# Optimization experiments

Hardware: AMD Instinct MI355X
Metric: run time of the kernel (lower is better)

Reference implementation:

```python
import jax, jax.numpy as jnp
import numpy as np

B, I, H = 4096, 512, 1024


def setup_inputs() -> dict:
    key = jax.random.key(0)
    ks = jax.random.split(key, 22)
    inp = {
        "y": jax.random.normal(ks[0], (B, I), jnp.float32),
        "h_light": jax.random.normal(ks[1], (B, H), jnp.float32),
        "c_light": jax.random.normal(ks[2], (B, H), jnp.float32),
        "h_temp": jax.random.normal(ks[3], (B, H), jnp.float32),
        "c_temp": jax.random.normal(ks[4], (B, H), jnp.float32),
    }
    names = ["w_f_light", "w_i_light", "w_c_light", "w_o_light",
             "w_f_light_temp", "w_i_light_temp", "w_c_light_temp", "w_o_light_temp"]
    for j, n in enumerate(names):
        inp[n] = jax.random.normal(ks[5 + j], (H, H + I), jnp.float32) * 0.02
        inp["b" + n[1:]] = jax.random.normal(ks[13 + j], (H,), jnp.float32) * 0.02
    return inp


def _branch(hx, wf, bf, wi, bi, wc, bc, wo, bo):
    # Fuse the 4 gate GEMMs of one branch into a single [B, H+I] x [H+I, 4H] matmul
    W = jnp.concatenate([wf, wi, wc, wo], axis=0)            # [4H, H+I]
    b = jnp.concatenate([bf, bi, bc, bo], axis=0)            # [4H]
    z = hx @ W.T + b                                         # [B, 4H]
    zf, zi, zc, zo = jnp.split(z, 4, axis=1)
    return jax.nn.sigmoid(zf), jax.nn.sigmoid(zi), jnp.tanh(zc), jax.nn.sigmoid(zo)


def reference(y, h_light, c_light, h_temp, c_temp,
              w_f_light, b_f_light, w_i_light, b_i_light,
              w_c_light, b_c_light, w_o_light, b_o_light,
              w_f_light_temp, b_f_light_temp, w_i_light_temp, b_i_light_temp,
              w_c_light_temp, b_c_light_temp, w_o_light_temp, b_o_light_temp):
    hx_l = jnp.concatenate([h_light, y], axis=1)  # [B, H+I]
    hx_t = jnp.concatenate([h_temp, y], axis=1)   # [B, H+I]
    f1, i1, ch1, o1 = _branch(hx_l, w_f_light, b_f_light, w_i_light, b_i_light,
                              w_c_light, b_c_light, w_o_light, b_o_light)
    f2, i2, ch2, o2 = _branch(hx_t, w_f_light_temp, b_f_light_temp, w_i_light_temp,
                              b_i_light_temp, w_c_light_temp, b_c_light_temp,
                              w_o_light_temp, b_o_light_temp)
    c_new = (f1 * c_light + i1 * ch1) + (f2 * c_light + i2 * ch2)
    h_new = (o1 + o2) * jnp.tanh(c_new)
    return h_new, c_new
```

## Files before the change

kernel.cpp:

```cpp
#include <hip/hip_runtime.h>
#include <stdint.h>


#define B_DIM 4096
#define I_DIM 512
#define H_DIM 1024
#define K_DIM 1536

typedef __attribute__((ext_vector_type(8))) __bf16 bf16x8;
typedef __attribute__((ext_vector_type(4))) float f32x4;
typedef __attribute__((ext_vector_type(4))) uint32_t u32x4;

static __device__ __forceinline__ uint32_t f2bf(float f) {
  uint32_t u = __builtin_bit_cast(uint32_t, f);
  return (u + 0x7FFFu + ((u >> 16) & 1u)) >> 16;
}
static __device__ __forceinline__ uint32_t pack2(float lo, float hi) {
  return f2bf(lo) | (f2bf(hi) << 16);
}
static __device__ __forceinline__ float sigf(float x) {
  return 1.f / (1.f + __expf(-x));
}
static __device__ __forceinline__ float tanhfast(float x) {
  float t = __expf(fminf(2.f * x, 80.f));
  return (t - 1.f) / (t + 1.f);
}

__global__ __launch_bounds__(256) void convert_kernel(
    const float* __restrict__ y, const float* __restrict__ h_light,
    const float* __restrict__ h_temp,
    const float* __restrict__ w0, const float* __restrict__ w1,
    const float* __restrict__ w2, const float* __restrict__ w3,
    const float* __restrict__ w4, const float* __restrict__ w5,
    const float* __restrict__ w6, const float* __restrict__ w7,
    uint16_t* __restrict__ ws)
{
  const int CPR = K_DIM / 8;
  const int A_CHUNKS = 2 * B_DIM * CPR;
  const int TOT = A_CHUNKS + 8 * H_DIM * CPR;
  for (int chunk = blockIdx.x * 256 + threadIdx.x; chunk < TOT;
       chunk += gridDim.x * 256) {
    int row_all = chunk / CPR;
    int cs = chunk - row_all * CPR;
    int cl = (cs & ~7) | ((cs & 7) ^ (row_all & 7));
    int k0 = cl * 8;
    const float* src;
    if (chunk < A_CHUNKS) {
      int branch = row_all >> 12;
      int row = row_all & (B_DIM - 1);
      const float* hb = branch ? h_temp : h_light;
      src = (k0 < H_DIM) ? (hb + (size_t)row * H_DIM + k0)
                         : (y + (size_t)row * I_DIM + (k0 - H_DIM));
    } else {
      int ra = row_all - 2 * B_DIM;
      int mat = ra >> 10;
      int row = ra & (H_DIM - 1);
      const float* w = (mat < 4) ? ((mat < 2) ? (mat == 0 ? w0 : w1) : (mat == 2 ? w2 : w3))
                                 : ((mat < 6) ? (mat == 4 ? w4 : w5) : (mat == 6 ? w6 : w7));
      src = w + (size_t)row * K_DIM + k0;
    }
    f32x4 v0 = *(const f32x4*)src;
    f32x4 v1 = *(const f32x4*)(src + 4);
    u32x4 o;
    o[0] = pack2(v0[0], v0[1]);
    o[1] = pack2(v0[2], v0[3]);
    o[2] = pack2(v1[0], v1[1]);
    o[3] = pack2(v1[2], v1[3]);
    *(u32x4*)(ws + (size_t)chunk * 8) = o;
  }
}

__global__ __launch_bounds__(512, 2) void lstm_fused_kernel(
    const uint16_t* __restrict__ ws,
    const float* __restrict__ c_light,
    const float* __restrict__ bf1, const float* __restrict__ bi1,
    const float* __restrict__ bc1, const float* __restrict__ bo1,
    const float* __restrict__ bf2, const float* __restrict__ bi2,
    const float* __restrict__ bc2, const float* __restrict__ bo2,
    float* __restrict__ out)
{
  __shared__ alignas(128) char smem[96 * 1024];

  const int tid = threadIdx.x;
  const int lane = tid & 63;
  const int wv = tid >> 6;

  int bid = blockIdx.x;
  int wg = (bid & 7) * 64 + (bid >> 3);
  const int bm0 = (wg >> 4) * 128;
  const int bn0 = (wg & 15) * 64;

  const uint16_t* wsA = ws;
  const uint16_t* wsW = ws + (size_t)2 * B_DIM * K_DIM;

  const int rA = lane & 15;
  const int kg = lane >> 4;
  const int swz = rA & 7;
  const int branch = wv >> 2;
  const char* As = smem + branch * 16384;
  const char* Bs = smem + 32768 + wv * 8192;

  f32x4 acc[8][4];
#pragma unroll
  for (int m = 0; m < 8; ++m)
#pragma unroll
    for (int n = 0; n < 4; ++n) acc[m][n] = (f32x4){0.f, 0.f, 0.f, 0.f};

  for (int kt = 0; kt < K_DIM / 64; ++kt) {
    __syncthreads();
#pragma unroll
    for (int i = 0; i < 12; ++i) {
      int chunk = i * 512 + tid;
      const uint16_t* src;
      if (chunk < 2048) {
        int br = chunk >> 10;
        int r = (chunk >> 3) & 127;
        int c = chunk & 7;
        src = wsA + (size_t)br * (B_DIM * K_DIM) + (size_t)(bm0 + r) * K_DIM + kt * 64 + c * 8;
      } else {
        int cb2 = chunk - 2048;
        int mt = cb2 >> 9;
        int r = (cb2 >> 3) & 63;
        int c = cb2 & 7;
        src = wsW + (size_t)mt * (H_DIM * K_DIM) + (size_t)(bn0 + r) * K_DIM + kt * 64 + c * 8;
      }
      __builtin_amdgcn_global_load_lds(
          (const __attribute__((address_space(1))) void*)src,
          (__attribute__((address_space(3))) void*)(smem + chunk * 16),
          16, 0, 0);
    }
    asm volatile("s_waitcnt vmcnt(0)" ::: "memory");
    __syncthreads();

#pragma unroll
    for (int kk = 0; kk < 2; ++kk) {
      const int cs = (kk * 4 + kg) ^ swz;
      bf16x8 a[8];
      bf16x8 b[4];
#pragma unroll
      for (int m = 0; m < 8; ++m)
        a[m] = *(const bf16x8*)(As + (m * 16 + rA) * 128 + cs * 16);
#pragma unroll
      for (int n = 0; n < 4; ++n)
        b[n] = *(const bf16x8*)(Bs + (n * 16 + rA) * 128 + cs * 16);
#pragma unroll
      for (int m = 0; m < 8; ++m)
#pragma unroll
        for (int n = 0; n < 4; ++n)
          acc[m][n] = __builtin_amdgcn_mfma_f32_16x16x32_bf16(a[m], b[n], acc[m][n], 0, 0, 0);
    }
  }

  float* zst = (float*)smem;
#pragma unroll
  for (int q = 0; q < 4; ++q) {
    __syncthreads();
#pragma unroll
    for (int mm = 0; mm < 2; ++mm)
#pragma unroll
      for (int n = 0; n < 4; ++n)
#pragma unroll
        for (int j = 0; j < 4; ++j) {
          int r = mm * 16 + kg * 4 + j;
          int c = n * 16 + rA;
          zst[wv * 2176 + r * 68 + c] = acc[q * 2 + mm][n][j];
        }
    __syncthreads();

    int r = tid >> 4;
    int cb = (tid & 15) * 4;
    int grow = bm0 + q * 32 + r;
    int gc = bn0 + cb;
    const float* zb = zst + r * 68 + cb;
    f32x4 z0 = *(const f32x4*)(zb + 0 * 2176) + *(const f32x4*)(bf1 + gc);
    f32x4 z1 = *(const f32x4*)(zb + 1 * 2176) + *(const f32x4*)(bi1 + gc);
    f32x4 z2 = *(const f32x4*)(zb + 2 * 2176) + *(const f32x4*)(bc1 + gc);
    f32x4 z3 = *(const f32x4*)(zb + 3 * 2176) + *(const f32x4*)(bo1 + gc);
    f32x4 z4 = *(const f32x4*)(zb + 4 * 2176) + *(const f32x4*)(bf2 + gc);
    f32x4 z5 = *(const f32x4*)(zb + 5 * 2176) + *(const f32x4*)(bi2 + gc);
    f32x4 z6 = *(const f32x4*)(zb + 6 * 2176) + *(const f32x4*)(bc2 + gc);
    f32x4 z7 = *(const f32x4*)(zb + 7 * 2176) + *(const f32x4*)(bo2 + gc);
    f32x4 cl4 = *(const f32x4*)(c_light + (size_t)grow * H_DIM + gc);
    f32x4 hv, cv;
#pragma unroll
    for (int j = 0; j < 4; ++j) {
      float f1 = sigf(z0[j]);
      float i1 = sigf(z1[j]);
      float ch1 = tanhfast(z2[j]);
      float o1 = sigf(z3[j]);
      float f2 = sigf(z4[j]);
      float i2 = sigf(z5[j]);
      float ch2 = tanhfast(z6[j]);
      float o2 = sigf(z7[j]);
      float cn = f1 * cl4[j] + i1 * ch1 + f2 * cl4[j] + i2 * ch2;
      hv[j] = (o1 + o2) * tanhfast(cn);
      cv[j] = cn;
    }
    *(f32x4*)(out + (size_t)grow * H_DIM + gc) = hv;
    *(f32x4*)(out + (size_t)(B_DIM * H_DIM) + (size_t)grow * H_DIM + gc) = cv;
  }
}

extern "C" void kernel_launch(void* const* d_in, const int* in_sizes, int n_in,
                              void* d_out, int out_size, void* d_ws, size_t ws_size,
                              hipStream_t stream) {
  (void)in_sizes; (void)n_in; (void)out_size; (void)ws_size;
  const float* y       = (const float*)d_in[0];
  const float* h_light = (const float*)d_in[1];
  const float* c_light = (const float*)d_in[2];
  const float* h_temp  = (const float*)d_in[3];
  uint16_t* ws = (uint16_t*)d_ws;

  convert_kernel<<<2048, 256, 0, stream>>>(
      y, h_light, h_temp,
      (const float*)d_in[5],  (const float*)d_in[7],  (const float*)d_in[9],  (const float*)d_in[11],
      (const float*)d_in[13], (const float*)d_in[15], (const float*)d_in[17], (const float*)d_in[19],
      ws);

  lstm_fused_kernel<<<512, 512, 0, stream>>>(
      ws, c_light,
      (const float*)d_in[6],  (const float*)d_in[8],  (const float*)d_in[10], (const float*)d_in[12],
      (const float*)d_in[14], (const float*)d_in[16], (const float*)d_in[18], (const float*)d_in[20],
      (float*)d_out);
}
```

Baseline: 328.1 us.

## Triple-buffer K tiles with interleaved async prefetch and split MFMA phases

The GEMM main loop now uses a 3-stage LDS ring with 32-wide K tiles. Prefetch loads for tile kt+2 are spread across two MFMA phases, and barriers plus s_setprio are used so loads overlap compute, replacing the old load-all, wait, then compute loop. The LDS swizzle is changed to match the 64-byte row layout. The convert kernel is simplified to one block per row with 192 threads. The extra LDS buffer (144KB total) and more barriers per tile may reduce occupancy relative to the launch bound of two blocks.

Result: faster. 303.1 us (-7.6%).

```diff
diff --git a/kernel.cpp b/kernel.cpp
--- a/kernel.cpp
+++ b/kernel.cpp
@@ -6,6 +6,8 @@
 #define I_DIM 512
 #define H_DIM 1024
 #define K_DIM 1536
+#define NK 48
+#define BUFB (48 * 1024)
 
 typedef __attribute__((ext_vector_type(8))) __bf16 bf16x8;
 typedef __attribute__((ext_vector_type(4))) float f32x4;
@@ -26,7 +28,7 @@
   return (t - 1.f) / (t + 1.f);
 }
 
-__global__ __launch_bounds__(256) void convert_kernel(
+__global__ __launch_bounds__(192) void convert_kernel(
     const float* __restrict__ y, const float* __restrict__ h_light,
     const float* __restrict__ h_temp,
     const float* __restrict__ w0, const float* __restrict__ w1,
@@ -35,39 +37,33 @@
     const float* __restrict__ w6, const float* __restrict__ w7,
     uint16_t* __restrict__ ws)
 {
-  const int CPR = K_DIM / 8;
-  const int A_CHUNKS = 2 * B_DIM * CPR;
-  const int TOT = A_CHUNKS + 8 * H_DIM * CPR;
-  for (int chunk = blockIdx.x * 256 + threadIdx.x; chunk < TOT;
-       chunk += gridDim.x * 256) {
-    int row_all = chunk / CPR;
-    int cs = chunk - row_all * CPR;
-    int cl = (cs & ~7) | ((cs & 7) ^ (row_all & 7));
-    int k0 = cl * 8;
-    const float* src;
-    if (chunk < A_CHUNKS) {
-      int branch = row_all >> 12;
-      int row = row_all & (B_DIM - 1);
-      const float* hb = branch ? h_temp : h_light;
-      src = (k0 < H_DIM) ? (hb + (size_t)row * H_DIM + k0)
-                         : (y + (size_t)row * I_DIM + (k0 - H_DIM));
-    } else {
-      int ra = row_all - 2 * B_DIM;
-      int mat = ra >> 10;
-      int row = ra & (H_DIM - 1);
-      const float* w = (mat < 4) ? ((mat < 2) ? (mat == 0 ? w0 : w1) : (mat == 2 ? w2 : w3))
-                                 : ((mat < 6) ? (mat == 4 ? w4 : w5) : (mat == 6 ? w6 : w7));
-      src = w + (size_t)row * K_DIM + k0;
-    }
-    f32x4 v0 = *(const f32x4*)src;
-    f32x4 v1 = *(const f32x4*)(src + 4);
-    u32x4 o;
-    o[0] = pack2(v0[0], v0[1]);
-    o[1] = pack2(v0[2], v0[3]);
-    o[2] = pack2(v1[0], v1[1]);
-    o[3] = pack2(v1[2], v1[3]);
-    *(u32x4*)(ws + (size_t)chunk * 8) = o;
-  }
+  const int row_all = blockIdx.x;
+  const int cs = threadIdx.x;
+  const int cl = (cs & ~3) | ((cs & 3) ^ ((row_all >> 1) & 3));
+  const int k0 = cl * 8;
+  const float* src;
+  if (row_all < 2 * B_DIM) {
+    const int branch = row_all >> 12;
+    const int row = row_all & (B_DIM - 1);
+    const float* hb = branch ? h_temp : h_light;
+    src = (k0 < H_DIM) ? (hb + (size_t)row * H_DIM + k0)
+                       : (y + (size_t)row * I_DIM + (k0 - H_DIM));
+  } else {
+    const int ra = row_all - 2 * B_DIM;
+    const int mat = ra >> 10;
+    const int row = ra & (H_DIM - 1);
+    const float* w = (mat < 4) ? ((mat < 2) ? (mat == 0 ? w0 : w1) : (mat == 2 ? w2 : w3))
+                               : ((mat < 6) ? (mat == 4 ? w4 : w5) : (mat == 6 ? w6 : w7));
+    src = w + (size_t)row * K_DIM + k0;
+  }
+  f32x4 v0 = *(const f32x4*)src;
+  f32x4 v1 = *(const f32x4*)(src + 4);
+  u32x4 o;
+  o[0] = pack2(v0[0], v0[1]);
+  o[1] = pack2(v0[2], v0[3]);
+  o[2] = pack2(v1[0], v1[1]);
+  o[3] = pack2(v1[2], v1[3]);
+  *(u32x4*)(ws + ((size_t)row_all * 192 + cs) * 8) = o;
 }
 
 __global__ __launch_bounds__(512, 2) void lstm_fused_kernel(
@@ -79,14 +75,14 @@
     const float* __restrict__ bc2, const float* __restrict__ bo2,
     float* __restrict__ out)
 {
-  __shared__ alignas(128) char smem[96 * 1024];
+  __shared__ alignas(128) char smem[3 * BUFB];
 
   const int tid = threadIdx.x;
   const int lane = tid & 63;
   const int wv = tid >> 6;
 
-  int bid = blockIdx.x;
-  int wg = (bid & 7) * 64 + (bid >> 3);
+  const int bid = blockIdx.x;
+  const int wg = (bid & 7) * 64 + (bid >> 3);
   const int bm0 = (wg >> 4) * 128;
   const int bn0 = (wg & 15) * 64;
 
@@ -95,10 +91,37 @@
 
   const int rA = lane & 15;
   const int kg = lane >> 4;
-  const int swz = rA & 7;
-  const int branch = wv >> 2;
-  const char* As = smem + branch * 16384;
-  const char* Bs = smem + 32768 + wv * 8192;
+  const uint32_t fo = (uint32_t)rA * 64u + (uint32_t)((kg ^ ((rA >> 1) & 3))) * 16u;
+
+  const uint16_t* sA0;
+  const uint16_t* sA1;
+  const uint16_t* sB[4];
+  {
+    int c = tid;
+    sA0 = wsA + (size_t)(bm0 + ((c >> 2) & 127)) * K_DIM + (c & 3) * 8;
+    c = 512 + tid;
+    sA1 = wsA + (size_t)B_DIM * K_DIM + (size_t)(bm0 + ((c >> 2) & 127)) * K_DIM + (c & 3) * 8;
+#pragma unroll
+    for (int j = 0; j < 4; ++j) {
+      int c2 = j * 512 + tid;
+      sB[j] = wsW + (size_t)(c2 >> 8) * ((size_t)H_DIM * K_DIM) +
+              (size_t)(bn0 + ((c2 >> 2) & 63)) * K_DIM + (c2 & 3) * 8;
+    }
+  }
+  const uint32_t ldA0 = (uint32_t)tid * 16u;
+  const uint32_t ldA1 = (uint32_t)(512 + tid) * 16u;
+  uint32_t ldB[4];
+#pragma unroll
+  for (int j = 0; j < 4; ++j) ldB[j] = (uint32_t)(1024 + j * 512 + tid) * 16u;
+
+  const uint32_t aBase = (uint32_t)(wv >> 2) * 8192u;
+  const uint32_t bBase = 16384u + (uint32_t)wv * 4096u;
+
+#define ISSUE(srcp, ldsoff, tg)                                              \
+  __builtin_amdgcn_global_load_lds(                                          \
+      (const __attribute__((address_space(1))) void*)(srcp),                 \
+      (__attribute__((address_space(3))) void*)(&smem[(size_t)(tg)*BUFB + (ldsoff)]), \
+      16, 0, 0)
 
   f32x4 acc[8][4];
 #pragma unroll
@@ -106,50 +129,64 @@
 #pragma unroll
     for (int n = 0; n < 4; ++n) acc[m][n] = (f32x4){0.f, 0.f, 0.f, 0.f};
 
-  for (int kt = 0; kt < K_DIM / 64; ++kt) {
-    __syncthreads();
-#pragma unroll
-    for (int i = 0; i < 12; ++i) {
-      int chunk = i * 512 + tid;
-      const uint16_t* src;
-      if (chunk < 2048) {
-        int br = chunk >> 10;
-        int r = (chunk >> 3) & 127;
-        int c = chunk & 7;
-        src = wsA + (size_t)br * (B_DIM * K_DIM) + (size_t)(bm0 + r) * K_DIM + kt * 64 + c * 8;
-      } else {
-        int cb2 = chunk - 2048;
-        int mt = cb2 >> 9;
-        int r = (cb2 >> 3) & 63;
-        int c = cb2 & 7;
-        src = wsW + (size_t)mt * (H_DIM * K_DIM) + (size_t)(bn0 + r) * K_DIM + kt * 64 + c * 8;
-      }
-      __builtin_amdgcn_global_load_lds(
-          (const __attribute__((address_space(1))) void*)src,
-          (__attribute__((address_space(3))) void*)(smem + chunk * 16),
-          16, 0, 0);
-    }
-    asm volatile("s_waitcnt vmcnt(0)" ::: "memory");
-    __syncthreads();
-
-#pragma unroll
-    for (int kk = 0; kk < 2; ++kk) {
-      const int cs = (kk * 4 + kg) ^ swz;
-      bf16x8 a[8];
-      bf16x8 b[4];
-#pragma unroll
-      for (int m = 0; m < 8; ++m)
-        a[m] = *(const bf16x8*)(As + (m * 16 + rA) * 128 + cs * 16);
+  ISSUE(sA0, ldA0, 0); ISSUE(sA1, ldA1, 0);
+#pragma unroll
+  for (int j = 0; j < 4; ++j) ISSUE(sB[j], ldB[j], 0);
+  ISSUE(sA0 + 32, ldA0, 1); ISSUE(sA1 + 32, ldA1, 1);
+#pragma unroll
+  for (int j = 0; j < 4; ++j) ISSUE(sB[j] + 32, ldB[j], 1);
+  sA0 += 64; sA1 += 64;
+#pragma unroll
+  for (int j = 0; j < 4; ++j) sB[j] += 64;
+  asm volatile("s_waitcnt vmcnt(6)" ::: "memory");
+  __builtin_amdgcn_s_barrier();
+
+  for (int kt = 0; kt < NK; ++kt) {
+    const int bi = kt % 3;
+    const int tg = (bi == 0) ? 2 : bi - 1;
+    const char* As = smem + (size_t)bi * BUFB + aBase;
+    const char* Bs = smem + (size_t)bi * BUFB + bBase;
+    const bool pf = (kt + 2 < NK);
+
+    bf16x8 Af[4], Bf[4];
+#pragma unroll
+    for (int m = 0; m < 4; ++m) Af[m] = *(const bf16x8*)(As + m * 1024 + fo);
+#pragma unroll
+    for (int n = 0; n < 4; ++n) Bf[n] = *(const bf16x8*)(Bs + n * 1024 + fo);
+    if (pf) { ISSUE(sA0, ldA0, tg); ISSUE(sA1, ldA1, tg); ISSUE(sB[0], ldB[0], tg); }
+    __builtin_amdgcn_s_barrier();
+    asm volatile("s_waitcnt lgkmcnt(0)" ::: "memory");
+    __builtin_amdgcn_s_setprio(1);
+#pragma unroll
+    for (int m = 0; m < 4; ++m)
 #pragma unroll
       for (int n = 0; n < 4; ++n)
-        b[n] = *(const bf16x8*)(Bs + (n * 16 + rA) * 128 + cs * 16);
-#pragma unroll
-      for (int m = 0; m < 8; ++m)
-#pragma unroll
-        for (int n = 0; n < 4; ++n)
-          acc[m][n] = __builtin_amdgcn_mfma_f32_16x16x32_bf16(a[m], b[n], acc[m][n], 0, 0, 0);
-    }
-  }
+        acc[m][n] = __builtin_amdgcn_mfma_f32_16x16x32_bf16(Af[m], Bf[n], acc[m][n], 0, 0, 0);
+    __builtin_amdgcn_s_setprio(0);
+    __builtin_amdgcn_s_barrier();
+
+    bf16x8 Ag[4];
+#pragma unroll
+    for (int m = 0; m < 4; ++m) Ag[m] = *(const bf16x8*)(As + (m + 4) * 1024 + fo);
+    if (pf) { ISSUE(sB[1], ldB[1], tg); ISSUE(sB[2], ldB[2], tg); ISSUE(sB[3], ldB[3], tg); }
+    __builtin_amdgcn_s_barrier();
+    asm volatile("s_waitcnt lgkmcnt(0)" ::: "memory");
+    __builtin_amdgcn_s_setprio(1);
+#pragma unroll
+    for (int m = 0; m < 4; ++m)
+#pragma unroll
+      for (int n = 0; n < 4; ++n)
+        acc[m + 4][n] = __builtin_amdgcn_mfma_f32_16x16x32_bf16(Ag[m], Bf[n], acc[m + 4][n], 0, 0, 0);
+    __builtin_amdgcn_s_setprio(0);
+    if (kt + 2 < NK) asm volatile("s_waitcnt vmcnt(6)" ::: "memory");
+    else             asm volatile("s_waitcnt vmcnt(0)" ::: "memory");
+    __builtin_amdgcn_s_barrier();
+
+    sA0 += 32; sA1 += 32;
+#pragma unroll
+    for (int j = 0; j < 4; ++j) sB[j] += 32;
+  }
+#undef ISSUE
 
   float* zst = (float*)smem;
 #pragma unroll
@@ -211,7 +248,7 @@
   const float* h_temp  = (const float*)d_in[3];
   uint16_t* ws = (uint16_t*)d_ws;
 
-  convert_kernel<<<2048, 256, 0, stream>>>(
+  convert_kernel<<<16384, 192, 0, stream>>>(
       y, h_light, h_temp,
       (const float*)d_in[5],  (const float*)d_in[7],  (const float*)d_in[9],  (const float*)d_in[11],
       (const float*)d_in[13], (const float*)d_in[15], (const float*)d_in[17], (const float*)d_in[19],
```
